# Kernel optimization log

Hardware: AMD Instinct MI355X
Metric: run time of the kernel (lower is better)

Reference implementation:

```python
import jax, jax.numpy as jnp
import numpy as np

DIM = 768
HEADS = 12
K_PARTS = 64
MLP_HIDDEN = 4 * DIM
EPS = 1e-5


def layer_norm(x, g, b):
    mu = jnp.mean(x, axis=-1, keepdims=True)
    var = jnp.mean(jnp.square(x - mu), axis=-1, keepdims=True)
    return (x - mu) * jax.lax.rsqrt(var + EPS) * g + b


def attention(x, qkv_w, qkv_b, proj_w, proj_b, num_heads):
    B, N, C = x.shape
    hd = C // num_heads
    scale = hd ** -0.5
    qkv = x @ qkv_w.T + qkv_b                      # (B,N,3C)
    qkv = qkv.reshape(B, N, 3, num_heads, hd).transpose(2, 0, 3, 1, 4)  # (3,B,H,N,hd)
    q, k, v = qkv[0], qkv[1], qkv[2]
    attn = jax.nn.softmax(jnp.einsum('bhqd,bhkd->bhqk', q, k) * scale, axis=-1)
    out = jnp.einsum('bhqk,bhkd->bhqd', attn, v)   # (B,H,N,hd)
    out = out.transpose(0, 2, 1, 3).reshape(B, N, C)
    return out @ proj_w.T + proj_b, attn


def mlp(x, fc1_w, fc1_b, fc2_w, fc2_b):
    h = jax.nn.gelu(x @ fc1_w.T + fc1_b, approximate=False)
    return h @ fc2_w.T + fc2_b


def setup_inputs() -> dict:
    key = jax.random.key(0)
    ks = jax.random.split(key, 16)
    s = lambda fan_in: 1.0 / np.sqrt(fan_in)
    inp = {
        'x': jax.random.normal(ks[0], (8, 1024, DIM), dtype=jnp.float32),
        'ln1_g': jnp.ones((DIM,), jnp.float32),
        'ln1_b': jnp.zeros((DIM,), jnp.float32),
        'qkv_w': jax.random.normal(ks[1], (3 * DIM, DIM), jnp.float32) * s(DIM),
        'qkv_b': jnp.zeros((3 * DIM,), jnp.float32),
        'proj_w': jax.random.normal(ks[2], (DIM, DIM), jnp.float32) * s(DIM),
        'proj_b': jnp.zeros((DIM,), jnp.float32),
        'c_qkv_w': jax.random.normal(ks[3], (3 * DIM, DIM), jnp.float32) * s(DIM),
        'c_qkv_b': jnp.zeros((3 * DIM,), jnp.float32),
        'c_proj_w': jax.random.normal(ks[4], (DIM, DIM), jnp.float32) * s(DIM),
        'c_proj_b': jnp.zeros((DIM,), jnp.float32),
        'cp_fc1_w': jax.random.normal(ks[5], (K_PARTS, K_PARTS), jnp.float32) * s(K_PARTS),
        'cp_fc1_b': jnp.zeros((K_PARTS,), jnp.float32),
        'cp_fc2_w': jax.random.normal(ks[6], (DIM, K_PARTS), jnp.float32) * s(K_PARTS),
        'cp_fc2_b': jnp.zeros((DIM,), jnp.float32),
        'P': jax.random.normal(ks[7], (K_PARTS, DIM), jnp.float32),
        'ln2_g': jnp.ones((DIM,), jnp.float32),
        'ln2_b': jnp.zeros((DIM,), jnp.float32),
        'fc1_w': jax.random.normal(ks[8], (MLP_HIDDEN, DIM), jnp.float32) * s(DIM),
        'fc1_b': jnp.zeros((MLP_HIDDEN,), jnp.float32),
        'fc2_w': jax.random.normal(ks[9], (DIM, MLP_HIDDEN), jnp.float32) * s(MLP_HIDDEN),
        'fc2_b': jnp.zeros((DIM,), jnp.float32),
    }
    # normalize P rows like the module init (F.normalize(orthogonal, dim=-1))
    inp['P'] = inp['P'] / jnp.linalg.norm(inp['P'], axis=-1, keepdims=True)
    return inp


def reference(x, ln1_g, ln1_b, qkv_w, qkv_b, proj_w, proj_b,
              c_qkv_w, c_qkv_b, c_proj_w, c_proj_b,
              cp_fc1_w, cp_fc1_b, cp_fc2_w, cp_fc2_b, P,
              ln2_g, ln2_b, fc1_w, fc1_b, fc2_w, fc2_b):
    n1 = layer_norm(x, ln1_g, ln1_b)
    y, _ = attention(n1, qkv_w, qkv_b, proj_w, proj_b, HEADS)
    # SimilarityMaps: L2-normalize tokens and parts, cosine similarity map (B,N,K)
    Un = n1 / jnp.linalg.norm(n1, axis=-1, keepdims=True)
    Pn = P / jnp.linalg.norm(P, axis=-1, keepdims=True)
    dmap = jnp.einsum('bnd,kd->bnk', Un, Pn)
    # c_project: Mlp K -> K -> dim, then parts attention
    zin = mlp(dmap, cp_fc1_w, cp_fc1_b, cp_fc2_w, cp_fc2_b)
    z, _ = attention(zin, c_qkv_w, c_qkv_b, c_proj_w, c_proj_b, HEADS)
    x = x + y + z                                  # gamma_1 is None, drop_path=0
    x = x + mlp(layer_norm(x, ln2_g, ln2_b), fc1_w, fc1_b, fc2_w, fc2_b)
    return x, dmap
```

## Files before the change

kernel.cpp:

```cpp
#include <hip/hip_runtime.h>


typedef unsigned short u16;
typedef unsigned int   u32;
typedef __attribute__((ext_vector_type(8))) short short8;
typedef __attribute__((ext_vector_type(8))) unsigned short ushort8v;
typedef __attribute__((ext_vector_type(4))) float f32x4;

#define F_GELU     1
#define F_ROWSCALE 2
#define F_RES1     4
#define F_RESF     8
#define F_OUTB     16
#define F_OUTF     32
#define F_BIAS     64

__device__ __forceinline__ float bf2f(u32 b) { return __uint_as_float(b << 16); }
__device__ __forceinline__ u16 f2bf(float f) {
    u32 u = __float_as_uint(f);
    u32 r = u + 0x7fffu + ((u >> 16) & 1u);
    return (u16)(r >> 16);
}
__device__ __forceinline__ u16 f2bf_fast(float f) {
    return (u16)((__float_as_uint(f) + 0x8000u) >> 16);
}
__device__ __forceinline__ float gelu_exact(float v) {
    return 0.5f * v * (1.0f + erff(v * 0.70710678118654752440f));
}
__device__ __forceinline__ float gelu_fast(float x) {
    float u = 0.79788456080286535588f * (x + 0.044715f * x * x * x);
    float e = __builtin_amdgcn_exp2f(u * 2.88539008177792681472f);
    float t = 1.0f - 2.0f / (e + 1.0f);
    return 0.5f * x * (1.0f + t);
}

__device__ __forceinline__ void gload16(const u16* g, u16* l) {
    __builtin_amdgcn_global_load_lds(
        (const __attribute__((address_space(1))) u32*)g,
        (__attribute__((address_space(3))) u32*)l, 16, 0, 0);
}

struct ConvArgs {
    const float* src[8];
    u16*         dst[8];
    int          nblk[9];
    int          n[8];
};

__global__ __launch_bounds__(256)
void conv_all_k(ConvArgs a)
{
    const int b = blockIdx.x;
    int i = 0;
    #pragma unroll
    for (int j = 0; j < 7; j++) if (b >= a.nblk[j + 1]) i = j + 1;
    const int base = (b - a.nblk[i]) * 1024 + threadIdx.x * 4;
    if (base >= a.n[i]) return;
    float4 v = *(const float4*)(a.src[i] + base);
    ushort4 o;
    o.x = f2bf(v.x); o.y = f2bf(v.y); o.z = f2bf(v.z); o.w = f2bf(v.w);
    *(ushort4*)(a.dst[i] + base) = o;
}

__device__ __forceinline__ float block_sum(float v, float* red) {
    #pragma unroll
    for (int off = 32; off > 0; off >>= 1) v += __shfl_down(v, off);
    __syncthreads();
    if ((threadIdx.x & 63) == 0) red[threadIdx.x >> 6] = v;
    __syncthreads();
    return red[0] + red[1] + red[2] + red[3];
}

template<bool NORM>
__global__ __launch_bounds__(256)
void ln_k(const float* __restrict__ xin, const float* __restrict__ g,
          const float* __restrict__ bta, u16* __restrict__ out,
          float* __restrict__ invnorm)
{
    __shared__ float red[4];
    const int row = blockIdx.x, t = threadIdx.x;
    float v[3];
    #pragma unroll
    for (int i = 0; i < 3; i++)
        v[i] = xin[(size_t)row * 768 + t + i * 256];
    float tot = block_sum(v[0] + v[1] + v[2], red);
    float mu  = tot * (1.0f / 768.0f);
    float d0 = v[0] - mu, d1 = v[1] - mu, d2 = v[2] - mu;
    float tot2 = block_sum(d0 * d0 + d1 * d1 + d2 * d2, red);
    float rstd = rsqrtf(tot2 * (1.0f / 768.0f) + 1e-5f);
    float ss = 0.0f;
    #pragma unroll
    for (int i = 0; i < 3; i++) {
        int c = t + i * 256;
        float yy = (v[i] - mu) * rstd * g[c] + bta[c];
        out[(size_t)row * 768 + c] = f2bf(yy);
        ss += yy * yy;
    }
    if constexpr (NORM) {
        float tot3 = block_sum(ss, red);
        if (t == 0) invnorm[row] = rsqrtf(tot3);
    }
}

__global__ __launch_bounds__(256)
void pn_k(const float* __restrict__ P, u16* __restrict__ Pn)
{
    __shared__ float red[4];
    const int row = blockIdx.x, t = threadIdx.x;
    float v[3];
    #pragma unroll
    for (int i = 0; i < 3; i++)
        v[i] = P[(size_t)row * 768 + t + i * 256];
    float tot = block_sum(v[0]*v[0] + v[1]*v[1] + v[2]*v[2], red);
    float inv = rsqrtf(tot);
    #pragma unroll
    for (int i = 0; i < 3; i++)
        Pn[(size_t)row * 768 + t + i * 256] = f2bf(v[i] * inv);
}

template<int FLAGS>
__global__ __launch_bounds__(512, 2)
void gemm256(const u16* __restrict__ A, const u16* __restrict__ W,
             const float* __restrict__ bias, u16* __restrict__ out,
             int M, int N, int K)
{
    __shared__ u16 As[2][16384];
    __shared__ u16 Bs[2][16384];
    const int t = threadIdx.x;
    const int wave = t >> 6, lane = t & 63;
    const int quad = lane >> 4, r16 = lane & 15;
    const int wr = wave >> 2, wc = wave & 3;

    const int nbx = gridDim.x, nby = gridDim.y;
    const int orig = blockIdx.x + blockIdx.y * nbx;
    const int Rc   = nby >> 3;
    const int xcd  = orig & 7, loc = orig >> 3;
    const int m0 = (xcd * Rc + (loc % Rc)) * 256;
    const int n0 = (loc / Rc) * 256;
    const int NT = K >> 6;

    f32x4 acc[8][4];
    #pragma unroll
    for (int i = 0; i < 8; i++)
        #pragma unroll
        for (int j = 0; j < 4; j++)
            acc[i][j] = (f32x4){0.f, 0.f, 0.f, 0.f};

    const int srow = wave * 8 + (lane >> 3);
    const int scol = ((lane & 7) ^ ((lane >> 3) & 7)) * 8;

    const u16* Abase = A + (size_t)m0 * K;
    const u16* Wbase = W + (size_t)n0 * K;

    #pragma unroll
    for (int i = 0; i < 4; i++)
        gload16(Abase + (size_t)(i * 64 + srow) * K + scol,
                &As[0][i * 4096 + wave * 512]);
    #pragma unroll
    for (int i = 0; i < 4; i++)
        gload16(Wbase + (size_t)(i * 64 + srow) * K + scol,
                &Bs[0][i * 4096 + wave * 512]);
    if (NT > 1) {
        #pragma unroll
        for (int i = 0; i < 4; i++)
            gload16(Abase + (size_t)(i * 64 + srow) * K + 64 + scol,
                    &As[1][i * 4096 + wave * 512]);
        #pragma unroll
        for (int i = 0; i < 4; i++)
            gload16(Wbase + (size_t)(i * 64 + srow) * K + 64 + scol,
                    &Bs[1][i * 4096 + wave * 512]);
    }

    for (int kt = 0; kt < NT; kt++) {
        const int c = kt & 1;
        if (kt + 1 < NT)
            asm volatile("s_waitcnt vmcnt(8)\n\ts_barrier" ::: "memory");
        else
            asm volatile("s_waitcnt vmcnt(0)\n\ts_barrier" ::: "memory");

        #pragma unroll
        for (int ks = 0; ks < 2; ks++) {
            short8 bfr[4], af[8];
            #pragma unroll
            for (int j = 0; j < 4; j++) {
                const int br = wc * 64 + j * 16 + r16;
                bfr[j] = *(const short8*)
                    &Bs[c][br * 64 + (((ks * 4 + quad) ^ (br & 7)) * 8)];
            }
            #pragma unroll
            for (int i = 0; i < 8; i++) {
                const int ar = wr * 128 + i * 16 + r16;
                af[i] = *(const short8*)
                    &As[c][ar * 64 + (((ks * 4 + quad) ^ (ar & 7)) * 8)];
            }
            __builtin_amdgcn_s_setprio(1);
            #pragma unroll
            for (int i = 0; i < 8; i++)
                #pragma unroll
                for (int j = 0; j < 4; j++)
                    acc[i][j] = __builtin_amdgcn_mfma_f32_16x16x32_bf16(
                        af[i], bfr[j], acc[i][j], 0, 0, 0);
            __builtin_amdgcn_s_setprio(0);
        }
        asm volatile("s_barrier" ::: "memory");
        if (kt + 2 < NT) {
            const int k0 = (kt + 2) * 64;
            #pragma unroll
            for (int i = 0; i < 4; i++)
                gload16(Abase + (size_t)(i * 64 + srow) * K + k0 + scol,
                        &As[c][i * 4096 + wave * 512]);
            #pragma unroll
            for (int i = 0; i < 4; i++)
                gload16(Wbase + (size_t)(i * 64 + srow) * K + k0 + scol,
                        &Bs[c][i * 4096 + wave * 512]);
        }
    }

    float* myl = (float*)&As[0][0] + wave * 1088;
    float bj[4];
    #pragma unroll
    for (int j = 0; j < 4; j++) {
        if constexpr (FLAGS & F_BIAS) bj[j] = bias[n0 + wc * 64 + j * 16 + r16];
        else bj[j] = 0.0f;
    }
    const int row = lane >> 2, seg = (lane & 3) * 16;

    #pragma unroll
    for (int i = 0; i < 8; i++) {
        #pragma unroll
        for (int j = 0; j < 4; j++)
            #pragma unroll
            for (int r = 0; r < 4; r++) {
                float v = acc[i][j][r] + bj[j];
                if constexpr (FLAGS & F_GELU) v = gelu_fast(v);
                myl[(quad * 4 + r) * 68 + j * 16 + r16] = v;
            }
        float v[16];
        #pragma unroll
        for (int k4 = 0; k4 < 4; k4++) {
            float4 f = *(const float4*)&myl[row * 68 + seg + k4 * 4];
            v[k4 * 4 + 0] = f.x; v[k4 * 4 + 1] = f.y;
            v[k4 * 4 + 2] = f.z; v[k4 * 4 + 3] = f.w;
        }
        const int m = m0 + wr * 128 + i * 16 + row;
        const size_t idx = (size_t)m * N + n0 + wc * 64 + seg;
        ushort8v o0, o1;
        #pragma unroll
        for (int k = 0; k < 8; k++) { o0[k] = f2bf(v[k]); o1[k] = f2bf(v[k + 8]); }
        *(ushort8v*)(out + idx) = o0;
        *(ushort8v*)(out + idx + 8) = o1;
    }
}

template<int FLAGS>
__global__ __launch_bounds__(256)
void gemm_mfma(const u16* __restrict__ A, const u16* __restrict__ W,
               const float* __restrict__ bias,
               const u16* __restrict__ res1, const float* __restrict__ resf,
               u16* __restrict__ out, float* __restrict__ outf,
               int M, int N, int K)
{
    __shared__ u16 smem[3][8192];
    const int t = threadIdx.x;
    const int wave = t >> 6, lane = t & 63;
    const int nbx  = gridDim.x;
    const int orig = blockIdx.x + blockIdx.y * nbx;
    const int cpx  = (nbx * gridDim.y) >> 3;
    const int xcd  = orig & 7, loc = orig >> 3;
    const int Rc   = cpx / nbx;
    const int gsz  = 6 * Rc;
    const int grp  = loc / gsz;
    const int rem  = loc - grp * gsz;
    const int ccol = grp * 6 + rem % 6;
    const int crow = xcd * Rc + rem / 6;
    const int m0 = crow * 128, n0 = ccol * 128;
    const int Wm = (wave >> 1) * 64, Wn = (wave & 1) * 64;
    const int rr = lane >> 2, cc = (lane & 3) * 8;
    const int quad = lane >> 4, r16 = lane & 15;
    const int NK = K >> 5;

    f32x4 acc[4][4];
    #pragma unroll
    for (int i = 0; i < 4; i++)
        #pragma unroll
        for (int j = 0; j < 4; j++)
            acc[i][j] = (f32x4){0.f, 0.f, 0.f, 0.f};

    #pragma unroll
    for (int c = 0; c < 2; c++) {
        const int chunk = wave * 2 + c;
        const int row = chunk * 16 + rr;
        gload16(A + (size_t)(m0 + row) * K + cc, &smem[0][chunk * 512]);
        gload16(W + (size_t)(n0 + row) * K + cc, &smem[0][4096 + chunk * 512]);
    }
    if (NK > 1) {
        #pragma unroll
        for (int c = 0; c < 2; c++) {
            const int chunk = wave * 2 + c;
            const int row = chunk * 16 + rr;
            gload16(A + (size_t)(m0 + row) * K + 32 + cc, &smem[1][chunk * 512]);
            gload16(W + (size_t)(n0 + row) * K + 32 + cc, &smem[1][4096 + chunk * 512]);
        }
    }

    for (int kt = 0; kt < NK; kt++) {
        const int cur = kt % 3;
        if (kt + 1 < NK)
            asm volatile("s_waitcnt vmcnt(4)\n\ts_barrier" ::: "memory");
        else
            asm volatile("s_waitcnt vmcnt(0)\n\ts_barrier" ::: "memory");
        if (kt + 2 < NK) {
            const int k0 = (kt + 2) * 32;
            const int nb = (kt + 2) % 3;
            #pragma unroll
            for (int c = 0; c < 2; c++) {
                const int chunk = wave * 2 + c;
                const int row = chunk * 16 + rr;
                gload16(A + (size_t)(m0 + row) * K + k0 + cc,
                        &smem[nb][chunk * 512]);
                gload16(W + (size_t)(n0 + row) * K + k0 + cc,
                        &smem[nb][4096 + chunk * 512]);
            }
        }
        short8 af[4], bfr[4];
        #pragma unroll
        for (int i = 0; i < 4; i++) {
            af[i]  = *(const short8*)&smem[cur][(Wm + i * 16 + r16) * 32 + quad * 8];
            bfr[i] = *(const short8*)&smem[cur][4096 + (Wn + i * 16 + r16) * 32 + quad * 8];
        }
        #pragma unroll
        for (int i = 0; i < 4; i++)
            #pragma unroll
            for (int j = 0; j < 4; j++)
                acc[i][j] = __builtin_amdgcn_mfma_f32_16x16x32_bf16(
                    af[i], bfr[j], acc[i][j], 0, 0, 0);
    }
    __syncthreads();

    float* myl = (float*)&smem[0][0] + wave * 1088;
    float bj[4];
    #pragma unroll
    for (int j = 0; j < 4; j++) {
        if constexpr (FLAGS & F_BIAS) bj[j] = bias[n0 + Wn + j * 16 + r16];
        else bj[j] = 0.0f;
    }
    const int row = lane >> 2, seg = (lane & 3) * 16;

    #pragma unroll
    for (int i = 0; i < 4; i++) {
        #pragma unroll
        for (int j = 0; j < 4; j++)
            #pragma unroll
            for (int r = 0; r < 4; r++) {
                float v = acc[i][j][r] + bj[j];
                if constexpr (FLAGS & F_GELU) v = gelu_fast(v);
                myl[(quad * 4 + r) * 68 + j * 16 + r16] = v;
            }
        float v[16];
        #pragma unroll
        for (int k4 = 0; k4 < 4; k4++) {
            float4 f = *(const float4*)&myl[row * 68 + seg + k4 * 4];
            v[k4 * 4 + 0] = f.x; v[k4 * 4 + 1] = f.y;
            v[k4 * 4 + 2] = f.z; v[k4 * 4 + 3] = f.w;
        }
        const int m = m0 + Wm + i * 16 + row;
        const size_t idx = (size_t)m * N + n0 + Wn + seg;
        if constexpr (FLAGS & F_RES1) {
            ushort8v r0 = *(const ushort8v*)(res1 + idx);
            ushort8v r1 = *(const ushort8v*)(res1 + idx + 8);
            #pragma unroll
            for (int k = 0; k < 8; k++) { v[k] += bf2f(r0[k]); v[k + 8] += bf2f(r1[k]); }
        }
        if constexpr (FLAGS & F_RESF) {
            #pragma unroll
            for (int k4 = 0; k4 < 4; k4++) {
                float4 f = *(const float4*)(resf + idx + k4 * 4);
                v[k4 * 4 + 0] += f.x; v[k4 * 4 + 1] += f.y;
                v[k4 * 4 + 2] += f.z; v[k4 * 4 + 3] += f.w;
            }
        }
        if constexpr (FLAGS & F_OUTB) {
            ushort8v o0, o1;
            #pragma unroll
            for (int k = 0; k < 8; k++) { o0[k] = f2bf(v[k]); o1[k] = f2bf(v[k + 8]); }
            *(ushort8v*)(out + idx) = o0;
            *(ushort8v*)(out + idx + 8) = o1;
        }
        if constexpr (FLAGS & F_OUTF) {
            #pragma unroll
            for (int k4 = 0; k4 < 4; k4++) {
                float4 f = {v[k4 * 4 + 0], v[k4 * 4 + 1], v[k4 * 4 + 2], v[k4 * 4 + 3]};
                *(float4*)(outf + idx + k4 * 4) = f;
            }
        }
    }
}

template<int BM, int BN, int FLAGS>
__global__ __launch_bounds__(256)
void gemm_k(const u16* __restrict__ A, const u16* __restrict__ W,
            const float* __restrict__ bias, const float* __restrict__ rowscale,
            const u16* __restrict__ res1, const float* __restrict__ resf,
            u16* __restrict__ out, float* __restrict__ outf,
            int M, int N, int K)
{
    constexpr int RM = BM / 16, RN = BN / 16;
    __shared__ float Asm[16][BM + 4];
    __shared__ float Wsm[16][BN + 4];
    const int t  = threadIdx.x;
    const int tx = t & 15, ty = t >> 4;
    const int m0 = blockIdx.y * BM, n0 = blockIdx.x * BN;

    float acc[RM][RN];
    #pragma unroll
    for (int i = 0; i < RM; i++)
        #pragma unroll
        for (int j = 0; j < RN; j++) acc[i][j] = 0.0f;

    for (int k0 = 0; k0 < K; k0 += 16) {
        #pragma unroll
        for (int i = 0; i < BM / 64; i++) {
            int f = t + i * 256, r = f >> 2, c4 = (f & 3) << 2;
            uint2 u = *(const uint2*)(A + (size_t)(m0 + r) * K + k0 + c4);
            Asm[c4 + 0][r] = bf2f(u.x & 0xffffu);
            Asm[c4 + 1][r] = bf2f(u.x >> 16);
            Asm[c4 + 2][r] = bf2f(u.y & 0xffffu);
            Asm[c4 + 3][r] = bf2f(u.y >> 16);
        }
        #pragma unroll
        for (int i = 0; i < BN / 64; i++) {
            int f = t + i * 256, r = f >> 2, c4 = (f & 3) << 2;
            uint2 u = *(const uint2*)(W + (size_t)(n0 + r) * K + k0 + c4);
            Wsm[c4 + 0][r] = bf2f(u.x & 0xffffu);
            Wsm[c4 + 1][r] = bf2f(u.x >> 16);
            Wsm[c4 + 2][r] = bf2f(u.y & 0xffffu);
            Wsm[c4 + 3][r] = bf2f(u.y >> 16);
        }
        __syncthreads();
        #pragma unroll
        for (int k = 0; k < 16; k++) {
            float a[RM], w[RN];
            #pragma unroll
            for (int ii = 0; ii < RM; ii += 4) {
                float4 v = *(const float4*)&Asm[k][ty * RM + ii];
                a[ii] = v.x; a[ii + 1] = v.y; a[ii + 2] = v.z; a[ii + 3] = v.w;
            }
            #pragma unroll
            for (int jj = 0; jj < RN; jj += 4) {
                float4 v = *(const float4*)&Wsm[k][tx * RN + jj];
                w[jj] = v.x; w[jj + 1] = v.y; w[jj + 2] = v.z; w[jj + 3] = v.w;
            }
            #pragma unroll
            for (int i = 0; i < RM; i++)
                #pragma unroll
                for (int j = 0; j < RN; j++)
                    acc[i][j] = fmaf(a[i], w[j], acc[i][j]);
        }
        __syncthreads();
    }

    #pragma unroll
    for (int i = 0; i < RM; i++) {
        const int m = m0 + ty * RM + i;
        float rs = 1.0f;
        if constexpr (FLAGS & F_ROWSCALE) rs = rowscale[m];
        #pragma unroll
        for (int jj = 0; jj < RN; jj += 4) {
            const int n = n0 + tx * RN + jj;
            const size_t idx = (size_t)m * N + n;
            float b4[4] = {0.f, 0.f, 0.f, 0.f};
            if constexpr (FLAGS & F_BIAS) {
                float4 bvv = *(const float4*)(bias + n);
                b4[0] = bvv.x; b4[1] = bvv.y; b4[2] = bvv.z; b4[3] = bvv.w;
            }
            float e[4];
            #pragma unroll
            for (int j = 0; j < 4; j++) {
                float v = acc[i][jj + j];
                if constexpr (FLAGS & F_BIAS) v += b4[j];
                if constexpr (FLAGS & F_GELU) v = gelu_exact(v);
                if constexpr (FLAGS & F_ROWSCALE) v *= rs;
                e[j] = v;
            }
            if constexpr (FLAGS & F_OUTB) {
                ushort4 o4;
                o4.x = f2bf(e[0]); o4.y = f2bf(e[1]);
                o4.z = f2bf(e[2]); o4.w = f2bf(e[3]);
                *(ushort4*)(out + idx) = o4;
            }
            if constexpr (FLAGS & F_OUTF) {
                float4 o4 = {e[0], e[1], e[2], e[3]};
                *(float4*)(outf + idx) = o4;
            }
        }
    }
}

__global__ __launch_bounds__(256)
void attn_mfma(const u16* __restrict__ qkv, u16* __restrict__ out)
{
    const int orig = blockIdx.x + blockIdx.y * 8;
    const int wg   = (orig & 7) * 96 + (orig >> 3);
    const int qt = wg & 7;
    const int bh = wg >> 3;
    const int b = bh / 12, h = bh % 12;
    __shared__ u16 Qs[2 * 128 * 32];
    __shared__ u16 Ks[2 * 64 * 32];
    __shared__ u16 Vt[2 * 64 * 32];
    __shared__ u16 Ps[2 * 128 * 32];
    const int t = threadIdx.x;
    const int wave = t >> 6, lane = t & 63;
    const int quad = lane >> 4, r16 = lane & 15;
    const size_t RS = 2304;
    const int tok0 = b * 1024 + qt * 128;
    const u16* qbase = qkv + (size_t)tok0 * RS + h * 64;
    const float SC = 0.125f * 1.44269504088896340736f;

    #pragma unroll
    for (int c = 0; c < 4; c++) {
        int idx = wave * 4 + c;
        int kc = idx >> 3, rg = idx & 7;
        int row = rg * 16 + (lane >> 2);
        gload16(qbase + (size_t)row * RS + kc * 32 + (lane & 3) * 8,
                &Qs[kc * 4096 + rg * 512]);
    }

    f32x4 O[2][4];
    float lpart[2][4];
    #pragma unroll
    for (int i = 0; i < 2; i++)
        #pragma unroll
        for (int j = 0; j < 4; j++) {
            O[i][j] = (f32x4){0.f, 0.f, 0.f, 0.f};
            lpart[i][j & 3] = 0.0f;
        }

    const int kp = t & 63, dg = t >> 6;
    const int vb = (kp >> 5) * 2048 + (kp & 31);
    uint2 vr[4];

    {
        const u16* kbase = qkv + (size_t)(b * 1024) * RS + 768 + h * 64;
        #pragma unroll
        for (int c = 0; c < 2; c++) {
            int idx = wave * 2 + c;
            int kc = idx >> 2, rg = idx & 3;
            int row = rg * 16 + (lane >> 2);
            gload16(kbase + (size_t)row * RS + kc * 32 + (lane & 3) * 8,
                    &Ks[kc * 2048 + rg * 512]);
        }
        const u16* vbase = qkv + (size_t)(b * 1024) * RS + 1536 + h * 64;
        #pragma unroll
        for (int it = 0; it < 4; it++) {
            int d0 = dg * 16 + it * 4;
            vr[it] = *(const uint2*)(vbase + (size_t)kp * RS + d0);
        }
    }

    for (int kt = 0; kt < 16; kt++) {
        __syncthreads();
        #pragma unroll
        for (int it = 0; it < 4; it++) {
            int d0 = dg * 16 + it * 4;
            uint2 u = vr[it];
            Vt[vb + (d0 + 0) * 32] = (u16)(u.x & 0xffffu);
            Vt[vb + (d0 + 1) * 32] = (u16)(u.x >> 16);
            Vt[vb + (d0 + 2) * 32] = (u16)(u.y & 0xffffu);
            Vt[vb + (d0 + 3) * 32] = (u16)(u.y >> 16);
        }

        f32x4 S[2][4];
        #pragma unroll
        for (int i = 0; i < 2; i++)
            #pragma unroll
            for (int j = 0; j < 4; j++)
                S[i][j] = (f32x4){0.f, 0.f, 0.f, 0.f};
        __builtin_amdgcn_s_setprio(1);
        #pragma unroll
        for (int kc = 0; kc < 2; kc++) {
            short8 aq[2], bk[4];
            #pragma unroll
            for (int i = 0; i < 2; i++)
                aq[i] = *(const short8*)&Qs[kc * 4096 + (wave * 32 + i * 16 + r16) * 32 + quad * 8];
            #pragma unroll
            for (int j = 0; j < 4; j++)
                bk[j] = *(const short8*)&Ks[kc * 2048 + (j * 16 + r16) * 32 + quad * 8];
            #pragma unroll
            for (int i = 0; i < 2; i++)
                #pragma unroll
                for (int j = 0; j < 4; j++)
                    S[i][j] = __builtin_amdgcn_mfma_f32_16x16x32_bf16(
                        aq[i], bk[j], S[i][j], 0, 0, 0);
        }
        __builtin_amdgcn_s_setprio(0);

        #pragma unroll
        for (int i = 0; i < 2; i++) {
            #pragma unroll
            for (int j = 0; j < 4; j++) {
                const int col = j * 16 + r16;
                const int pb = (col >> 5) * 4096 + (col & 31);
                #pragma unroll
                for (int r = 0; r < 4; r++) {
                    float p = __builtin_amdgcn_exp2f(S[i][j][r] * SC);
                    lpart[i][r] += p;
                    const int row = wave * 32 + i * 16 + quad * 4 + r;
                    Ps[pb + row * 32] = f2bf_fast(p);
                }
            }
        }

        __syncthreads();

        if (kt < 15) {
            const u16* kbase = qkv + (size_t)(b * 1024 + (kt + 1) * 64) * RS + 768 + h * 64;
            #pragma unroll
            for (int c = 0; c < 2; c++) {
                int idx = wave * 2 + c;
                int kc = idx >> 2, rg = idx & 3;
                int row = rg * 16 + (lane >> 2);
                gload16(kbase + (size_t)row * RS + kc * 32 + (lane & 3) * 8,
                        &Ks[kc * 2048 + rg * 512]);
            }
            const u16* vbase = qkv + (size_t)(b * 1024 + (kt + 1) * 64) * RS + 1536 + h * 64;
            #pragma unroll
            for (int it = 0; it < 4; it++) {
                int d0 = dg * 16 + it * 4;
                vr[it] = *(const uint2*)(vbase + (size_t)kp * RS + d0);
            }
        }

        __builtin_amdgcn_s_setprio(1);
        #pragma unroll
        for (int kc = 0; kc < 2; kc++) {
            short8 ap[2], bv[4];
            #pragma unroll
            for (int i = 0; i < 2; i++)
                ap[i] = *(const short8*)&Ps[kc * 4096 + (wave * 32 + i * 16 + r16) * 32 + quad * 8];
            #pragma unroll
            for (int j = 0; j < 4; j++)
                bv[j] = *(const short8*)&Vt[kc * 2048 + (j * 16 + r16) * 32 + quad * 8];
            #pragma unroll
            for (int i = 0; i < 2; i++)
                #pragma unroll
                for (int j = 0; j < 4; j++)
                    O[i][j] = __builtin_amdgcn_mfma_f32_16x16x32_bf16(
                        ap[i], bv[j], O[i][j], 0, 0, 0);
        }
        __builtin_amdgcn_s_setprio(0);
    }

    const int row = lane >> 2, seg = (lane & 3) * 16;
    #pragma unroll
    for (int i = 0; i < 2; i++) {
        float linv[4];
        #pragma unroll
        for (int r = 0; r < 4; r++) {
            float l = lpart[i][r];
            l += __shfl_xor(l, 1);
            l += __shfl_xor(l, 2);
            l += __shfl_xor(l, 4);
            l += __shfl_xor(l, 8);
            linv[r] = 1.0f / l;
        }
        u16* myl = &Ps[wave * 2048 + i * 1024];
        #pragma unroll
        for (int j = 0; j < 4; j++)
            #pragma unroll
            for (int r = 0; r < 4; r++)
                myl[(quad * 4 + r) * 64 + j * 16 + r16] = f2bf(O[i][j][r] * linv[r]);
        const int token = tok0 + wave * 32 + i * 16 + row;
        const size_t oidx = (size_t)token * 768 + h * 64 + seg;
        *(ushort8v*)(out + oidx)     = *(const ushort8v*)&myl[row * 64 + seg];
        *(ushort8v*)(out + oidx + 8) = *(const ushort8v*)&myl[row * 64 + seg + 8];
    }
}

extern "C" void kernel_launch(void* const* d_in, const int* in_sizes, int n_in,
                              void* d_out, int out_size, void* d_ws, size_t ws_size,
                              hipStream_t stream)
{
    (void)in_sizes; (void)n_in; (void)out_size; (void)ws_size;
    const float* x        = (const float*)d_in[0];
    const float* ln1_g    = (const float*)d_in[1];
    const float* ln1_b    = (const float*)d_in[2];
    const float* qkv_w    = (const float*)d_in[3];
    const float* qkv_b    = (const float*)d_in[4];
    const float* proj_w   = (const float*)d_in[5];
    const float* proj_b   = (const float*)d_in[6];
    const float* c_qkv_w  = (const float*)d_in[7];
    const float* c_qkv_b  = (const float*)d_in[8];
    const float* c_proj_w = (const float*)d_in[9];
    const float* c_proj_b = (const float*)d_in[10];
    const float* cp_fc1_w = (const float*)d_in[11];
    const float* cp_fc1_b = (const float*)d_in[12];
    const float* cp_fc2_w = (const float*)d_in[13];
    const float* cp_fc2_b = (const float*)d_in[14];
    const float* P        = (const float*)d_in[15];
    const float* ln2_g    = (const float*)d_in[16];
    const float* ln2_b    = (const float*)d_in[17];
    const float* fc1_w    = (const float*)d_in[18];
    const float* fc1_b    = (const float*)d_in[19];
    const float* fc2_w    = (const float*)d_in[20];
    const float* fc2_b    = (const float*)d_in[21];

    float* out_x    = (float*)d_out;
    float* out_dmap = out_x + 6291456;

    u16* us    = (u16*)d_ws;
    u16* n1n2  = us;
    u16* bigA  = us + 6291456;
    u16* ao    = bigA + 18874368;
    u16* y     = us + 31457280;
    float* xs  = (float*)(us + 37748736);
    u16* dmapb = us + 50331648;
    u16* cph   = us + 50855936;
    u16* Pn    = us + 51380224;
    float* invn = (float*)(us + 51429376);
    u16* ci    = us + 51445760;

    u16* w_qkv   = ci;
    u16* w_proj  = ci + 1769472;
    u16* w_cqkv  = ci + 2359296;
    u16* w_cproj = ci + 4128768;
    u16* w_cpf1  = ci + 4718592;
    u16* w_cpf2  = ci + 4722688;
    u16* w_fc1   = ci + 4771840;
    u16* w_fc2   = ci + 7131136;

    {
        ConvArgs a;
        const float* wsrc[8] = { qkv_w, proj_w, c_qkv_w, c_proj_w,
                                 cp_fc1_w, cp_fc2_w, fc1_w, fc2_w };
        u16* wdst[8] = { w_qkv, w_proj, w_cqkv, w_cproj,
                         w_cpf1, w_cpf2, w_fc1, w_fc2 };
        const int wn[8] = { 1769472, 589824, 1769472, 589824,
                            4096, 49152, 2359296, 2359296 };
        int cum = 0;
        for (int i = 0; i < 8; i++) {
            a.src[i] = wsrc[i]; a.dst[i] = wdst[i]; a.n[i] = wn[i];
            a.nblk[i] = cum;
            cum += (wn[i] / 4 + 255) / 256;
        }
        a.nblk[8] = cum;
        conv_all_k<<<cum, 256, 0, stream>>>(a);
    }

    pn_k<<<64, 256, 0, stream>>>(P, Pn);
    ln_k<true><<<8192, 256, 0, stream>>>(x, ln1_g, ln1_b, n1n2, invn);
    gemm256<F_BIAS | F_OUTB>
        <<<dim3(9, 32), 512, 0, stream>>>(n1n2, w_qkv, qkv_b, bigA,
                                          8192, 2304, 768);
    attn_mfma<<<dim3(8, 96), 256, 0, stream>>>(bigA, ao);
    gemm_mfma<F_BIAS | F_OUTB>
        <<<dim3(6, 64), 256, 0, stream>>>(ao, w_proj, proj_b, nullptr, nullptr,
                                          y, nullptr, 8192, 768, 768);
    gemm_k<64, 64, F_ROWSCALE | F_OUTB | F_OUTF>
        <<<dim3(1, 128), 256, 0, stream>>>(n1n2, Pn, nullptr, invn, nullptr,
                                           nullptr, dmapb, out_dmap, 8192, 64, 768);
    gemm_k<64, 64, F_BIAS | F_GELU | F_OUTB>
        <<<dim3(1, 128), 256, 0, stream>>>(dmapb, w_cpf1, cp_fc1_b, nullptr,
                                           nullptr, nullptr, cph, nullptr, 8192, 64, 64);
    gemm_mfma<F_BIAS | F_OUTB>
        <<<dim3(6, 64), 256, 0, stream>>>(cph, w_cpf2, cp_fc2_b, nullptr, nullptr,
                                          n1n2, nullptr, 8192, 768, 64);
    gemm256<F_BIAS | F_OUTB>
        <<<dim3(9, 32), 512, 0, stream>>>(n1n2, w_cqkv, c_qkv_b, bigA,
                                          8192, 2304, 768);
    attn_mfma<<<dim3(8, 96), 256, 0, stream>>>(bigA, ao);
    gemm_mfma<F_BIAS | F_RES1 | F_RESF | F_OUTF>
        <<<dim3(6, 64), 256, 0, stream>>>(ao, w_cproj, c_proj_b, y, x,
                                          nullptr, xs, 8192, 768, 768);
    ln_k<false><<<8192, 256, 0, stream>>>(xs, ln2_g, ln2_b, n1n2, nullptr);
    gemm256<F_BIAS | F_GELU | F_OUTB>
        <<<dim3(12, 32), 512, 0, stream>>>(n1n2, w_fc1, fc1_b, bigA,
                                           8192, 3072, 768);
    gemm_mfma<F_BIAS | F_RESF | F_OUTF>
        <<<dim3(6, 64), 256, 0, stream>>>(bigA, w_fc2, fc2_b, nullptr, xs,
                                          nullptr, out_x, 8192, 768, 3072);
}
```

Baseline: 588.3 us.

## Interleave next-tile global loads with MFMA phases in 256x256 GEMM main loop

Restructures the GEMM K-loop from a two-tile-ahead prefetch issued after compute into a one-tile-ahead scheme. Each K-tile is split into four quarter phases, and the next tile's A/B halves are staged across those phases between LDS reads and MFMA bursts. The goal is to spread global-to-LDS traffic over the compute and cut register pressure by loading fewer A fragments at a time. In exchange it adds two barriers per quarter phase and shortens prefetch lead time to a single tile, which may expose load latency.

```diff
diff --git a/kernel.cpp b/kernel.cpp
--- a/kernel.cpp
+++ b/kernel.cpp
@@ -152,67 +152,66 @@
     const u16* Abase = A + (size_t)m0 * K;
     const u16* Wbase = W + (size_t)n0 * K;
 
-    #pragma unroll
-    for (int i = 0; i < 4; i++)
-        gload16(Abase + (size_t)(i * 64 + srow) * K + scol,
-                &As[0][i * 4096 + wave * 512]);
-    #pragma unroll
-    for (int i = 0; i < 4; i++)
-        gload16(Wbase + (size_t)(i * 64 + srow) * K + scol,
-                &Bs[0][i * 4096 + wave * 512]);
-    if (NT > 1) {
-        #pragma unroll
-        for (int i = 0; i < 4; i++)
-            gload16(Abase + (size_t)(i * 64 + srow) * K + 64 + scol,
-                    &As[1][i * 4096 + wave * 512]);
-        #pragma unroll
-        for (int i = 0; i < 4; i++)
-            gload16(Wbase + (size_t)(i * 64 + srow) * K + 64 + scol,
-                    &Bs[1][i * 4096 + wave * 512]);
-    }
-
+    auto stage_half = [&](int h, int kt, int e) {
+        const int k0 = kt * 64;
+        const u16* g = (h < 2) ? (Abase + (size_t)((h & 1) * 128) * K)
+                               : (Wbase + (size_t)((h & 1) * 128) * K);
+        u16* l = (h < 2) ? &As[e][(h & 1) * 8192] : &Bs[e][(h & 1) * 8192];
+        #pragma unroll
+        for (int i = 0; i < 2; i++)
+            gload16(g + (size_t)(i * 64 + srow) * K + k0 + scol,
+                    l + i * 4096 + wave * 512);
+    };
+
+    #pragma unroll
+    for (int h = 0; h < 4; h++) stage_half(h, 0, 0);
+    asm volatile("s_waitcnt vmcnt(0)" ::: "memory");
+    __syncthreads();
+
+    short8 bfr[2][4];
     for (int kt = 0; kt < NT; kt++) {
-        const int c = kt & 1;
-        if (kt + 1 < NT)
-            asm volatile("s_waitcnt vmcnt(8)\n\ts_barrier" ::: "memory");
-        else
-            asm volatile("s_waitcnt vmcnt(0)\n\ts_barrier" ::: "memory");
-
-        #pragma unroll
-        for (int ks = 0; ks < 2; ks++) {
-            short8 bfr[4], af[8];
-            #pragma unroll
-            for (int j = 0; j < 4; j++) {
-                const int br = wc * 64 + j * 16 + r16;
-                bfr[j] = *(const short8*)
-                    &Bs[c][br * 64 + (((ks * 4 + quad) ^ (br & 7)) * 8)];
-            }
-            #pragma unroll
-            for (int i = 0; i < 8; i++) {
-                const int ar = wr * 128 + i * 16 + r16;
-                af[i] = *(const short8*)
-                    &As[c][ar * 64 + (((ks * 4 + quad) ^ (ar & 7)) * 8)];
-            }
+        const int d = kt & 1, e = d ^ 1;
+        const bool pf = (kt + 1 < NT);
+        #pragma unroll
+        for (int q = 0; q < 4; q++) {
+            short8 af[2][2];
+            #pragma unroll
+            for (int ks = 0; ks < 2; ks++)
+                #pragma unroll
+                for (int ii = 0; ii < 2; ii++) {
+                    const int ar = wr * 128 + (q * 2 + ii) * 16 + r16;
+                    af[ks][ii] = *(const short8*)
+                        &As[d][ar * 64 + (((ks * 4 + quad) ^ (ar & 7)) * 8)];
+                }
+            if (q == 0) {
+                #pragma unroll
+                for (int ks = 0; ks < 2; ks++)
+                    #pragma unroll
+                    for (int j = 0; j < 4; j++) {
+                        const int br = wc * 64 + j * 16 + r16;
+                        bfr[ks][j] = *(const short8*)
+                            &Bs[d][br * 64 + (((ks * 4 + quad) ^ (br & 7)) * 8)];
+                    }
+            }
+            if (pf) {
+                if (q == 0) { stage_half(0, kt + 1, e); stage_half(1, kt + 1, e); }
+                else if (q == 1) stage_half(2, kt + 1, e);
+                else if (q == 2) stage_half(3, kt + 1, e);
+            }
+            if (q == 3)
+                asm volatile("s_waitcnt vmcnt(0)" ::: "memory");
+            asm volatile("s_barrier" ::: "memory");
             __builtin_amdgcn_s_setprio(1);
             #pragma unroll
-            for (int i = 0; i < 8; i++)
+            for (int ks = 0; ks < 2; ks++)
                 #pragma unroll
-                for (int j = 0; j < 4; j++)
-                    acc[i][j] = __builtin_amdgcn_mfma_f32_16x16x32_bf16(
-                        af[i], bfr[j], acc[i][j], 0, 0, 0);
+                for (int ii = 0; ii < 2; ii++)
+                    #pragma unroll
+                    for (int j = 0; j < 4; j++)
+                        acc[q * 2 + ii][j] = __builtin_amdgcn_mfma_f32_16x16x32_bf16(
+                            af[ks][ii], bfr[ks][j], acc[q * 2 + ii][j], 0, 0, 0);
             __builtin_amdgcn_s_setprio(0);
-        }
-        asm volatile("s_barrier" ::: "memory");
-        if (kt + 2 < NT) {
-            const int k0 = (kt + 2) * 64;
-            #pragma unroll
-            for (int i = 0; i < 4; i++)
-                gload16(Abase + (size_t)(i * 64 + srow) * K + k0 + scol,
-                        &As[c][i * 4096 + wave * 512]);
-            #pragma unroll
-            for (int i = 0; i < 4; i++)
-                gload16(Wbase + (size_t)(i * 64 + srow) * K + k0 + scol,
-                        &Bs[c][i * 4096 + wave * 512]);
+            asm volatile("s_barrier" ::: "memory");
         }
     }
 
```

New measurement: 579.8 us. No clear change (-1.4%).
